# Performance work log

Measured on AMD Instinct MI355X. Metric: run time of the kernel, lower is better.

The kernel has to match this reference:

```python
import jax, jax.numpy as jnp
import numpy as np

# LIF hyperparameters (match init_kwargs)
DT = 1.0
TAU = 20.0
THRESHOLD = 1.0
RESET = 0.0
REST = 0.0
REFR_PERIOD = 2.0
LOW_BOUND = -1.0
KOEFF = float(np.exp(-DT / TAU))  # membrane decay per step
N = 2048
N_IN = 512
N_OUT = 256
B = 64
T = 512


def setup_inputs() -> dict:
    key = jax.random.key(0)
    k1, k2 = jax.random.split(key)
    # Binary input spike trains [B, n_in, T] (uint8 semantics, stored as float32)
    inp = (jax.random.uniform(k1, (B, N_IN, T)) < 0.2).astype(jnp.float32)
    # Dense synaptic weight matrix W [N, N]; row i = incoming weights of neuron i
    W = jax.random.normal(k2, (N, N), dtype=jnp.float32) * (0.1 / np.sqrt(N))
    return {"inp": inp, "W": W}


def reference(inp, W):
    batch, n_in, time = inp.shape
    n = W.shape[0]
    xs = jnp.moveaxis(inp, 2, 0)  # [T, B, n_in]

    def step(carry, x_t):
        state, refr, out_t = carry  # state/refr/out_t: [B, N]
        # Inject input spikes into the first n_in output slots
        out_t = out_t.at[:, :n_in].set(x_t)
        # LIF update: decay toward rest + synaptic input W @ out_t
        state = (state - REST) * KOEFF + REST + jnp.einsum('ij,bj->bi', W, out_t)
        # Refractory neurons clamped to reset potential
        state = jnp.where(refr > 0, RESET, state)
        spike = state >= THRESHOLD
        refr = refr - DT
        refr = jnp.where(spike, REFR_PERIOD, refr)
        # Lower-bound clamp on membrane potential
        state = jnp.where(state < LOW_BOUND, LOW_BOUND, state)
        out_t = spike.astype(jnp.float32)
        return (state, refr, out_t), out_t[:, -N_OUT:]

    init = (jnp.zeros((batch, n), jnp.float32),
            jnp.zeros((batch, n), jnp.float32),
            jnp.zeros((batch, n), jnp.float32))
    _, outs = jax.lax.scan(step, init, xs)  # outs: [T, B, n_out]
    return jnp.transpose(outs, (1, 2, 0))  # [B, n_out, T]
```

## Files before the change

### kernel.cpp

```cpp
#include <hip/hip_runtime.h>

#define KOEFF 0.951229424500714f
#define K64   0.040762204f

typedef unsigned short u16;
typedef __attribute__((ext_vector_type(8))) short short8;
typedef __attribute__((ext_vector_type(4))) float f32x4;

__device__ __forceinline__ u16 f2bf(float f) {
  unsigned int v = __float_as_uint(f);
  unsigned int r = (v + 0x7FFFu + ((v >> 16) & 1u)) >> 16;
  return (u16)r;
}
__device__ __forceinline__ float bf2f(u16 u) {
  return __uint_as_float(((unsigned int)u) << 16);
}

__global__ __launch_bounds__(256) void k_xt(const float* __restrict__ X, u16* __restrict__ XT) {
  __shared__ float tile[64][65];
  const int b  = blockIdx.z;
  const int j0 = blockIdx.x * 64;
  const int t0 = blockIdx.y * 64;
  const float* src = X + ((size_t)b * 512 + j0) * 512 + t0;
  for (int e = threadIdx.x; e < 64 * 16; e += 256) {
    int r = e >> 4, c = e & 15;
    float4 v = *(const float4*)(src + (size_t)r * 512 + c * 4);
    tile[r][c * 4 + 0] = v.x; tile[r][c * 4 + 1] = v.y;
    tile[r][c * 4 + 2] = v.z; tile[r][c * 4 + 3] = v.w;
  }
  __syncthreads();
  u16* dst = XT + ((size_t)b * 512 + t0) * 512 + j0;
  for (int e = threadIdx.x; e < 64 * 16; e += 256) {
    int tr = e >> 4, c = e & 15;
    ushort4 o;
    o.x = f2bf(tile[c * 4 + 0][tr]); o.y = f2bf(tile[c * 4 + 1][tr]);
    o.z = f2bf(tile[c * 4 + 2][tr]); o.w = f2bf(tile[c * 4 + 3][tr]);
    *(ushort4*)(dst + (size_t)tr * 512 + c * 4) = o;
  }
}

__global__ __launch_bounds__(256) void k_wcvt(const float* __restrict__ W,
                                              u16* __restrict__ Whi, int* __restrict__ flags) {
  if (blockIdx.x == 0 && threadIdx.x < 64) flags[threadIdx.x] = 0;
  int p = blockIdx.x * 256 + threadIdx.x;
  if (p >= 1536 * 512) return;
  int i = p >> 9, j = p & 511;
  Whi[p] = f2bf(W[(size_t)(512 + i) * 2048 + j]);
}

__global__ __launch_bounds__(256) void k_wt2(const float* __restrict__ W, float* __restrict__ WT2) {
  __shared__ float tile[64][65];
  const int i0 = blockIdx.x * 64;
  const int j0 = blockIdx.y * 64;
  const float* src = W + (size_t)(512 + i0) * 2048 + 512 + j0;
  for (int e = threadIdx.x; e < 64 * 16; e += 256) {
    int r = e >> 4, c = e & 15;
    float4 v = *(const float4*)(src + (size_t)r * 2048 + c * 4);
    tile[r][c * 4 + 0] = v.x; tile[r][c * 4 + 1] = v.y;
    tile[r][c * 4 + 2] = v.z; tile[r][c * 4 + 3] = v.w;
  }
  __syncthreads();
  float* dst = WT2 + (size_t)j0 * 1536 + i0;
  for (int e = threadIdx.x; e < 64 * 16; e += 256) {
    int jr = e >> 4, c = e & 15;
    float4 o;
    o.x = tile[c * 4 + 0][jr]; o.y = tile[c * 4 + 1][jr];
    o.z = tile[c * 4 + 2][jr]; o.w = tile[c * 4 + 3][jr];
    *(float4*)(dst + (size_t)jr * 1536 + c * 4) = o;
  }
}

__global__ __launch_bounds__(256) void k_gemm(const u16* __restrict__ A,
                                              const u16* __restrict__ Bx, u16* __restrict__ U) {
  __shared__ u16 lA[128 * 64];
  __shared__ u16 lB[128 * 64];
  const int b    = blockIdx.y;
  const int mt   = blockIdx.x >> 2;
  const int nt   = blockIdx.x & 3;
  const int tid  = threadIdx.x;
  const int wv   = tid >> 6;
  const int lane = tid & 63;
  const int wr   = wv >> 1, wc = wv & 1;

  f32x4 acc[4][4];
#pragma unroll
  for (int mi = 0; mi < 4; ++mi)
#pragma unroll
    for (int ni = 0; ni < 4; ++ni) acc[mi][ni] = (f32x4)0.0f;

  const u16* gA = A + (size_t)mt * 128 * 512;
  const u16* gB = Bx + ((size_t)b * 512 + nt * 128) * 512;

  for (int k0 = 0; k0 < 512; k0 += 64) {
#pragma unroll
    for (int it = 0; it < 4; ++it) {
      int byteoff = wv * 4096 + it * 1024 + lane * 16;
      int row   = byteoff >> 7;
      int chunk = (byteoff >> 4) & 7;
      int ksub  = (chunk ^ (row & 7)) * 8;
      int ldsoff = wv * 2048 + it * 512;
      __builtin_amdgcn_global_load_lds(
          (const __attribute__((address_space(1))) void*)(gA + (size_t)row * 512 + k0 + ksub),
          (__attribute__((address_space(3))) void*)(lA + ldsoff), 16, 0, 0);
      __builtin_amdgcn_global_load_lds(
          (const __attribute__((address_space(1))) void*)(gB + (size_t)row * 512 + k0 + ksub),
          (__attribute__((address_space(3))) void*)(lB + ldsoff), 16, 0, 0);
    }
    __syncthreads();
#pragma unroll
    for (int kk = 0; kk < 2; ++kk) {
      short8 ah[4], bb[4];
      const int kc = kk * 4 + (lane >> 4);
      const int sw = lane & 7;
#pragma unroll
      for (int mi = 0; mi < 4; ++mi) {
        int m = wr * 64 + mi * 16 + (lane & 15);
        ah[mi] = *(const short8*)&lA[m * 64 + ((kc ^ sw) << 3)];
      }
#pragma unroll
      for (int ni = 0; ni < 4; ++ni) {
        int n = wc * 64 + ni * 16 + (lane & 15);
        bb[ni] = *(const short8*)&lB[n * 64 + ((kc ^ sw) << 3)];
      }
#pragma unroll
      for (int mi = 0; mi < 4; ++mi)
#pragma unroll
        for (int ni = 0; ni < 4; ++ni)
          acc[mi][ni] = __builtin_amdgcn_mfma_f32_16x16x32_bf16(ah[mi], bb[ni], acc[mi][ni], 0, 0, 0);
    }
    __syncthreads();
  }
#pragma unroll
  for (int mi = 0; mi < 4; ++mi) {
    int ib = mt * 128 + wr * 64 + mi * 16 + ((lane >> 4) << 2);
#pragma unroll
    for (int ni = 0; ni < 4; ++ni) {
      int t = nt * 128 + wc * 64 + ni * 16 + (lane & 15);
      f32x4 v = acc[mi][ni];
      ushort4 o;
      o.x = f2bf(v.x); o.y = f2bf(v.y); o.z = f2bf(v.z); o.w = f2bf(v.w);
      *(ushort4*)(U + ((size_t)b * 512 + t) * 1536 + ib) = o;
    }
  }
}

__global__ __launch_bounds__(256) void k_part(const u16* __restrict__ U, float* __restrict__ P) {
  const int g = blockIdx.x * 256 + threadIdx.x;
  const int i = g * 2;
  const int c = blockIdx.y, b = blockIdx.z;
  const u16* up = U + ((size_t)b * 512 + c * 64) * 1536 + i;
  float s0 = 0.f, s1 = 0.f;
  unsigned int buf[8];
#pragma unroll
  for (int j = 0; j < 8; ++j) buf[j] = *(const unsigned int*)(up + (size_t)j * 1536);
  for (int t0 = 0; t0 < 64; t0 += 8) {
#pragma unroll
    for (int j = 0; j < 8; ++j) {
      unsigned int u = buf[j];
      if (t0 + 8 < 64) buf[j] = *(const unsigned int*)(up + (size_t)(t0 + 8 + j) * 1536);
      s0 = fmaf(s0, KOEFF, bf2f((u16)(u & 0xffffu)));
      s1 = fmaf(s1, KOEFF, bf2f((u16)(u >> 16)));
    }
  }
  *(float2*)(P + ((size_t)b * 8 + c) * 1536 + i) = make_float2(s0, s1);
}

__global__ __launch_bounds__(256) void k_chunk(const u16* __restrict__ U, const float* __restrict__ P,
                                               float* __restrict__ out, int* __restrict__ flags) {
  const int g = blockIdx.x * 256 + threadIdx.x;
  const int i = g * 2;
  const int c = blockIdx.y, b = blockIdx.z;
  float s0 = 0.f, s1 = 0.f;
  const float* pp = P + (size_t)b * 8 * 1536 + i;
  for (int d = 0; d < c; ++d) {
    float2 pv = *(const float2*)(pp + (size_t)d * 1536);
    s0 = fmaf(s0, K64, pv.x);
    s1 = fmaf(s1, K64, pv.y);
  }
  const u16* up = U + ((size_t)b * 512 + c * 64) * 1536 + i;
  const bool wr = (i >= 1280);
  float* op = out + ((size_t)b * 256 + (i - 1280)) * 512 + c * 64;
  bool viol = false;
  unsigned int buf[8];
#pragma unroll
  for (int j = 0; j < 8; ++j) buf[j] = *(const unsigned int*)(up + (size_t)j * 1536);
  for (int t0 = 0; t0 < 64; t0 += 8) {
    float sp0[8], sp1[8];
#pragma unroll
    for (int j = 0; j < 8; ++j) {
      unsigned int u = buf[j];
      if (t0 + 8 < 64) buf[j] = *(const unsigned int*)(up + (size_t)(t0 + 8 + j) * 1536);
      s0 = fmaf(s0, KOEFF, bf2f((u16)(u & 0xffffu)));
      s1 = fmaf(s1, KOEFF, bf2f((u16)(u >> 16)));
      bool a = (s0 >= 1.0f), bsp = (s1 >= 1.0f);
      viol = viol || a || bsp || (s0 < -1.0f) || (s1 < -1.0f);
      sp0[j] = a ? 1.f : 0.f;
      sp1[j] = bsp ? 1.f : 0.f;
    }
    if (wr) {
      *(float4*)(op + t0)           = make_float4(sp0[0], sp0[1], sp0[2], sp0[3]);
      *(float4*)(op + t0 + 4)       = make_float4(sp0[4], sp0[5], sp0[6], sp0[7]);
      *(float4*)(op + 512 + t0)     = make_float4(sp1[0], sp1[1], sp1[2], sp1[3]);
      *(float4*)(op + 512 + t0 + 4) = make_float4(sp1[4], sp1[5], sp1[6], sp1[7]);
    }
  }
  if (viol) atomicOr(&flags[b], 1);
}

__global__ __launch_bounds__(768) void k_fix(const u16* __restrict__ U, const float* __restrict__ WT2,
                                             const int* __restrict__ flags, float* __restrict__ out) {
  const int b = blockIdx.x;
  if (flags[b] == 0) return;
  const int tid = threadIdx.x;
  const int wv = tid >> 6, lane = tid & 63;
  __shared__ unsigned long long spk[24];
  for (int w = tid; w < 24; w += 768) spk[w] = 0ULL;
  __syncthreads();
  float s0 = 0.f, s1 = 0.f, r0 = 0.f, r1 = 0.f;
  const int i0 = 2 * tid;
  const u16* ub = U + (size_t)b * 512 * 1536 + i0;
  unsigned int u = *(const unsigned int*)ub;
  for (int t = 0; t < 512; ++t) {
    unsigned int unext = u;
    if (t < 511) unext = *(const unsigned int*)(ub + (size_t)(t + 1) * 1536);
    float a0 = fmaf(s0, KOEFF, bf2f((u16)(u & 0xffffu)));
    float a1 = fmaf(s1, KOEFF, bf2f((u16)(u >> 16)));
    for (int wd = 0; wd < 24; ++wd) {
      unsigned long long m = spk[wd];
      while (m) {
        int bit = __ffsll(m) - 1;
        m &= m - 1;
        int jp = ((wd >> 1) << 7) + (bit << 1) + (wd & 1);
        float2 rv = *(const float2*)(WT2 + (size_t)jp * 1536 + i0);
        a0 += rv.x; a1 += rv.y;
      }
    }
    if (r0 > 0.f) a0 = 0.f;
    if (r1 > 0.f) a1 = 0.f;
    bool sp0 = a0 >= 1.0f, sp1 = a1 >= 1.0f;
    r0 -= 1.f; r1 -= 1.f;
    if (sp0) r0 = 2.f;
    if (sp1) r1 = 2.f;
    if (a0 < -1.f) a0 = -1.f;
    if (a1 < -1.f) a1 = -1.f;
    s0 = a0; s1 = a1;
    if (i0 >= 1280) {
      float* o = out + ((size_t)b * 256 + (i0 - 1280)) * 512 + t;
      o[0]   = sp0 ? 1.f : 0.f;
      o[512] = sp1 ? 1.f : 0.f;
    }
    __syncthreads();
    unsigned long long b0 = __ballot(sp0);
    unsigned long long b1 = __ballot(sp1);
    if (lane == 0) { spk[2 * wv] = b0; spk[2 * wv + 1] = b1; }
    __syncthreads();
    u = unext;
  }
}

__global__ __launch_bounds__(256) void k_wtf(const float* __restrict__ W, float* __restrict__ WTF) {
  __shared__ float tile[64][65];
  const int i0 = blockIdx.x * 64;
  const int j0 = blockIdx.y * 64;
  const float* src = W + (size_t)(512 + i0) * 2048 + j0;
  for (int e = threadIdx.x; e < 64 * 16; e += 256) {
    int r = e >> 4, c = e & 15;
    float4 v = *(const float4*)(src + (size_t)r * 2048 + c * 4);
    tile[r][c * 4 + 0] = v.x; tile[r][c * 4 + 1] = v.y;
    tile[r][c * 4 + 2] = v.z; tile[r][c * 4 + 3] = v.w;
  }
  __syncthreads();
  float* dst = WTF + (size_t)j0 * 1536 + i0;
  for (int e = threadIdx.x; e < 64 * 16; e += 256) {
    int jr = e >> 4, c = e & 15;
    float4 o;
    o.x = tile[c * 4 + 0][jr]; o.y = tile[c * 4 + 1][jr];
    o.z = tile[c * 4 + 2][jr]; o.w = tile[c * 4 + 3][jr];
    *(float4*)(dst + (size_t)jr * 1536 + c * 4) = o;
  }
}

__global__ __launch_bounds__(256) void k_exact(const float* __restrict__ X, const float* __restrict__ W,
                                               const float* __restrict__ WTF, int use_wt,
                                               float* __restrict__ out) {
  const int b = blockIdx.x, tid = threadIdx.x;
  const int wv = tid >> 6, lane = tid & 63;
  float st[6], rf[6];
#pragma unroll
  for (int r = 0; r < 6; ++r) { st[r] = 0.f; rf[r] = 0.f; }
  __shared__ unsigned int mask[64];
  for (int w = tid; w < 64; w += 256) mask[w] = 0u;
  __syncthreads();
  for (int t = 0; t < 512; ++t) {
    {
      float x = X[((size_t)b * 512 + tid) * 512 + t];
      unsigned long long bl = __ballot(x > 0.5f);
      if (lane == 0) { mask[2 * wv] = (unsigned int)bl; mask[2 * wv + 1] = (unsigned int)(bl >> 32); }
      x = X[((size_t)b * 512 + 256 + tid) * 512 + t];
      bl = __ballot(x > 0.5f);
      if (lane == 0) { mask[8 + 2 * wv] = (unsigned int)bl; mask[9 + 2 * wv] = (unsigned int)(bl >> 32); }
    }
    __syncthreads();
    float add[6] = {0.f, 0.f, 0.f, 0.f, 0.f, 0.f};
    for (int wd = 0; wd < 64; ++wd) {
      unsigned int m = mask[wd];
      while (m) {
        int bitp = __ffs(m) - 1;
        m &= m - 1;
        int j = wd * 32 + bitp;
        if (use_wt) {
          const float* row = WTF + (size_t)j * 1536;
#pragma unroll
          for (int r = 0; r < 6; ++r) add[r] += row[tid + 256 * r];
        } else {
#pragma unroll
          for (int r = 0; r < 6; ++r) add[r] += W[(size_t)(512 + tid + 256 * r) * 2048 + j];
        }
      }
    }
    bool sp[6];
#pragma unroll
    for (int r = 0; r < 6; ++r) {
      float a = fmaf(st[r], KOEFF, add[r]);
      if (rf[r] > 0.f) a = 0.f;
      sp[r] = a >= 1.0f;
      rf[r] -= 1.f;
      if (sp[r]) rf[r] = 2.f;
      if (a < -1.f) a = -1.f;
      st[r] = a;
      int gi = 512 + tid + 256 * r;
      if (gi >= 1792) out[((size_t)b * 256 + (gi - 1792)) * 512 + t] = sp[r] ? 1.f : 0.f;
    }
    __syncthreads();
#pragma unroll
    for (int r = 0; r < 6; ++r) {
      unsigned long long bl = __ballot(sp[r]);
      if (lane == 0) {
        mask[16 + 8 * r + 2 * wv] = (unsigned int)bl;
        mask[17 + 8 * r + 2 * wv] = (unsigned int)(bl >> 32);
      }
    }
    __syncthreads();
  }
}

extern "C" void kernel_launch(void* const* d_in, const int* in_sizes, int n_in,
                              void* d_out, int out_size, void* d_ws, size_t ws_size,
                              hipStream_t stream) {
  const float* X = (const float*)d_in[0];
  const float* W = (const float*)d_in[1];
  float* out = (float*)d_out;
  char* ws = (char*)d_ws;

  const size_t SZ_XT  = 64ull * 512 * 512 * 2;
  const size_t SZ_WH  = 1536ull * 512 * 2;
  const size_t SZ_WT2 = 1536ull * 1536 * 4;
  const size_t SZ_U   = 64ull * 512 * 1536 * 2;
  const size_t SZ_P   = 64ull * 8 * 1536 * 4;
  const size_t SZ_FL  = 256;
  const size_t NEED_FULL = SZ_XT + SZ_WH + SZ_WT2 + SZ_U + SZ_P + SZ_FL;
  const size_t NEED_MID  = 2048ull * 1536 * 4;

  if (ws_size >= NEED_FULL) {
    u16*   XT  = (u16*)ws;
    u16*   Whi = (u16*)(ws + SZ_XT);
    float* WT2 = (float*)(ws + SZ_XT + SZ_WH);
    u16*   U   = (u16*)(ws + SZ_XT + SZ_WH + SZ_WT2);
    float* P   = (float*)(ws + SZ_XT + SZ_WH + SZ_WT2 + SZ_U);
    int*   FL  = (int*)(ws + SZ_XT + SZ_WH + SZ_WT2 + SZ_U + SZ_P);
    k_xt<<<dim3(8, 8, 64), 256, 0, stream>>>(X, XT);
    k_wcvt<<<3072, 256, 0, stream>>>(W, Whi, FL);
    k_wt2<<<dim3(24, 24), 256, 0, stream>>>(W, WT2);
    k_gemm<<<dim3(48, 64), 256, 0, stream>>>(Whi, XT, U);
    k_part<<<dim3(3, 8, 64), 256, 0, stream>>>(U, P);
    k_chunk<<<dim3(3, 8, 64), 256, 0, stream>>>(U, P, out, FL);
    k_fix<<<64, 768, 0, stream>>>(U, WT2, FL, out);
  } else if (ws_size >= NEED_MID) {
    float* WTF = (float*)ws;
    k_wtf<<<dim3(24, 32), 256, 0, stream>>>(W, WTF);
    k_exact<<<64, 256, 0, stream>>>(X, W, WTF, 1, out);
  } else {
    k_exact<<<64, 256, 0, stream>>>(X, W, nullptr, 0, out);
  }
}
```

Measured before the change: 252.0 us.

## Fuse prep kernels into one launch and compute chunk partials in GEMM epilogue

Merges the three preprocessing kernels (input transpose, weight bf16 conversion, weight transpose) into a single launch that dispatches on block index. It also drops the separate partial-sum kernel: the GEMM epilogue computes each 64-step chunk's decayed sum directly from the fp32 accumulators, using exp2-based decay weights and a 16-lane shuffle reduction. This removes three launches and a full re-read of the bf16 U buffer. The trade-offs are a heavier GEMM epilogue and partials that now come from the fp32 accumulators instead of the rounded bf16 values, which slightly changes numerics.

Measured after the change: 237.4 us. -5.8%, faster.

```diff
diff --git a/kernel.cpp b/kernel.cpp
--- a/kernel.cpp
+++ b/kernel.cpp
@@ -2,6 +2,7 @@
 
 #define KOEFF 0.951229424500714f
 #define K64   0.040762204f
+#define LOG2K (-0.07213475204444817f)
 
 typedef unsigned short u16;
 typedef __attribute__((ext_vector_type(8))) short short8;
@@ -16,62 +17,63 @@
   return __uint_as_float(((unsigned int)u) << 16);
 }
 
-__global__ __launch_bounds__(256) void k_xt(const float* __restrict__ X, u16* __restrict__ XT) {
+__global__ __launch_bounds__(256) void k_prep(const float* __restrict__ X, const float* __restrict__ W,
+                                              u16* __restrict__ XT, u16* __restrict__ Whi,
+                                              float* __restrict__ WT2, int* __restrict__ flags) {
   __shared__ float tile[64][65];
-  const int b  = blockIdx.z;
-  const int j0 = blockIdx.x * 64;
-  const int t0 = blockIdx.y * 64;
-  const float* src = X + ((size_t)b * 512 + j0) * 512 + t0;
-  for (int e = threadIdx.x; e < 64 * 16; e += 256) {
-    int r = e >> 4, c = e & 15;
-    float4 v = *(const float4*)(src + (size_t)r * 512 + c * 4);
-    tile[r][c * 4 + 0] = v.x; tile[r][c * 4 + 1] = v.y;
-    tile[r][c * 4 + 2] = v.z; tile[r][c * 4 + 3] = v.w;
-  }
-  __syncthreads();
-  u16* dst = XT + ((size_t)b * 512 + t0) * 512 + j0;
-  for (int e = threadIdx.x; e < 64 * 16; e += 256) {
-    int tr = e >> 4, c = e & 15;
-    ushort4 o;
-    o.x = f2bf(tile[c * 4 + 0][tr]); o.y = f2bf(tile[c * 4 + 1][tr]);
-    o.z = f2bf(tile[c * 4 + 2][tr]); o.w = f2bf(tile[c * 4 + 3][tr]);
-    *(ushort4*)(dst + (size_t)tr * 512 + c * 4) = o;
-  }
-}
-
-__global__ __launch_bounds__(256) void k_wcvt(const float* __restrict__ W,
-                                              u16* __restrict__ Whi, int* __restrict__ flags) {
-  if (blockIdx.x == 0 && threadIdx.x < 64) flags[threadIdx.x] = 0;
-  int p = blockIdx.x * 256 + threadIdx.x;
-  if (p >= 1536 * 512) return;
-  int i = p >> 9, j = p & 511;
-  Whi[p] = f2bf(W[(size_t)(512 + i) * 2048 + j]);
-}
-
-__global__ __launch_bounds__(256) void k_wt2(const float* __restrict__ W, float* __restrict__ WT2) {
-  __shared__ float tile[64][65];
-  const int i0 = blockIdx.x * 64;
-  const int j0 = blockIdx.y * 64;
-  const float* src = W + (size_t)(512 + i0) * 2048 + 512 + j0;
-  for (int e = threadIdx.x; e < 64 * 16; e += 256) {
-    int r = e >> 4, c = e & 15;
-    float4 v = *(const float4*)(src + (size_t)r * 2048 + c * 4);
-    tile[r][c * 4 + 0] = v.x; tile[r][c * 4 + 1] = v.y;
-    tile[r][c * 4 + 2] = v.z; tile[r][c * 4 + 3] = v.w;
-  }
-  __syncthreads();
-  float* dst = WT2 + (size_t)j0 * 1536 + i0;
-  for (int e = threadIdx.x; e < 64 * 16; e += 256) {
-    int jr = e >> 4, c = e & 15;
-    float4 o;
-    o.x = tile[c * 4 + 0][jr]; o.y = tile[c * 4 + 1][jr];
-    o.z = tile[c * 4 + 2][jr]; o.w = tile[c * 4 + 3][jr];
-    *(float4*)(dst + (size_t)jr * 1536 + c * 4) = o;
+  const int blk = blockIdx.x;
+  if (blk < 4096) {
+    const int b  = blk >> 6;
+    const int r2 = blk & 63;
+    const int j0 = (r2 & 7) * 64;
+    const int t0 = (r2 >> 3) * 64;
+    const float* src = X + ((size_t)b * 512 + j0) * 512 + t0;
+    for (int e = threadIdx.x; e < 64 * 16; e += 256) {
+      int r = e >> 4, c = e & 15;
+      float4 v = *(const float4*)(src + (size_t)r * 512 + c * 4);
+      tile[r][c * 4 + 0] = v.x; tile[r][c * 4 + 1] = v.y;
+      tile[r][c * 4 + 2] = v.z; tile[r][c * 4 + 3] = v.w;
+    }
+    __syncthreads();
+    u16* dst = XT + ((size_t)b * 512 + t0) * 512 + j0;
+    for (int e = threadIdx.x; e < 64 * 16; e += 256) {
+      int tr = e >> 4, c = e & 15;
+      ushort4 o;
+      o.x = f2bf(tile[c * 4 + 0][tr]); o.y = f2bf(tile[c * 4 + 1][tr]);
+      o.z = f2bf(tile[c * 4 + 2][tr]); o.w = f2bf(tile[c * 4 + 3][tr]);
+      *(ushort4*)(dst + (size_t)tr * 512 + c * 4) = o;
+    }
+  } else if (blk < 7168) {
+    if (blk == 4096 && threadIdx.x < 64) flags[threadIdx.x] = 0;
+    int p = (blk - 4096) * 256 + threadIdx.x;
+    int i = p >> 9, j = p & 511;
+    Whi[p] = f2bf(W[(size_t)(512 + i) * 2048 + j]);
+  } else {
+    const int bx = blk - 7168;
+    const int i0 = (bx / 24) * 64;
+    const int j0 = (bx % 24) * 64;
+    const float* src = W + (size_t)(512 + i0) * 2048 + 512 + j0;
+    for (int e = threadIdx.x; e < 64 * 16; e += 256) {
+      int r = e >> 4, c = e & 15;
+      float4 v = *(const float4*)(src + (size_t)r * 2048 + c * 4);
+      tile[r][c * 4 + 0] = v.x; tile[r][c * 4 + 1] = v.y;
+      tile[r][c * 4 + 2] = v.z; tile[r][c * 4 + 3] = v.w;
+    }
+    __syncthreads();
+    float* dst = WT2 + (size_t)j0 * 1536 + i0;
+    for (int e = threadIdx.x; e < 64 * 16; e += 256) {
+      int jr = e >> 4, c = e & 15;
+      float4 o;
+      o.x = tile[c * 4 + 0][jr]; o.y = tile[c * 4 + 1][jr];
+      o.z = tile[c * 4 + 2][jr]; o.w = tile[c * 4 + 3][jr];
+      *(float4*)(dst + (size_t)jr * 1536 + c * 4) = o;
+    }
   }
 }
 
 __global__ __launch_bounds__(256) void k_gemm(const u16* __restrict__ A,
-                                              const u16* __restrict__ Bx, u16* __restrict__ U) {
+                                              const u16* __restrict__ Bx, u16* __restrict__ U,
+                                              float* __restrict__ P) {
   __shared__ u16 lA[128 * 64];
   __shared__ u16 lB[128 * 64];
   const int b    = blockIdx.y;
@@ -142,27 +144,42 @@
       *(ushort4*)(U + ((size_t)b * 512 + t) * 1536 + ib) = o;
     }
   }
-}
-
-__global__ __launch_bounds__(256) void k_part(const u16* __restrict__ U, float* __restrict__ P) {
-  const int g = blockIdx.x * 256 + threadIdx.x;
-  const int i = g * 2;
-  const int c = blockIdx.y, b = blockIdx.z;
-  const u16* up = U + ((size_t)b * 512 + c * 64) * 1536 + i;
-  float s0 = 0.f, s1 = 0.f;
-  unsigned int buf[8];
-#pragma unroll
-  for (int j = 0; j < 8; ++j) buf[j] = *(const unsigned int*)(up + (size_t)j * 1536);
-  for (int t0 = 0; t0 < 64; t0 += 8) {
-#pragma unroll
-    for (int j = 0; j < 8; ++j) {
-      unsigned int u = buf[j];
-      if (t0 + 8 < 64) buf[j] = *(const unsigned int*)(up + (size_t)(t0 + 8 + j) * 1536);
-      s0 = fmaf(s0, KOEFF, bf2f((u16)(u & 0xffffu)));
-      s1 = fmaf(s1, KOEFF, bf2f((u16)(u >> 16)));
-    }
-  }
-  *(float2*)(P + ((size_t)b * 8 + c) * 1536 + i) = make_float2(s0, s1);
+  {
+    const int tl = lane & 15;
+    const int c  = nt * 2 + wc;
+    float pv[4][4];
+#pragma unroll
+    for (int mi = 0; mi < 4; ++mi)
+#pragma unroll
+      for (int q = 0; q < 4; ++q) pv[mi][q] = 0.f;
+#pragma unroll
+    for (int ni = 0; ni < 4; ++ni) {
+      float w = exp2f(LOG2K * (float)(63 - ni * 16 - tl));
+#pragma unroll
+      for (int mi = 0; mi < 4; ++mi) {
+        f32x4 a = acc[mi][ni];
+        pv[mi][0] = fmaf(w, a.x, pv[mi][0]);
+        pv[mi][1] = fmaf(w, a.y, pv[mi][1]);
+        pv[mi][2] = fmaf(w, a.z, pv[mi][2]);
+        pv[mi][3] = fmaf(w, a.w, pv[mi][3]);
+      }
+    }
+#pragma unroll
+    for (int off = 1; off < 16; off <<= 1)
+#pragma unroll
+      for (int mi = 0; mi < 4; ++mi)
+#pragma unroll
+        for (int q = 0; q < 4; ++q)
+          pv[mi][q] += __shfl_xor(pv[mi][q], off, 16);
+    if (tl == 0) {
+      int ib = mt * 128 + wr * 64 + ((lane >> 4) << 2);
+      float* pb = P + ((size_t)b * 8 + c) * 1536 + ib;
+#pragma unroll
+      for (int mi = 0; mi < 4; ++mi)
+#pragma unroll
+        for (int q = 0; q < 4; ++q) pb[mi * 16 + q] = pv[mi][q];
+    }
+  }
 }
 
 __global__ __launch_bounds__(256) void k_chunk(const u16* __restrict__ U, const float* __restrict__ P,
@@ -368,11 +385,8 @@
     u16*   U   = (u16*)(ws + SZ_XT + SZ_WH + SZ_WT2);
     float* P   = (float*)(ws + SZ_XT + SZ_WH + SZ_WT2 + SZ_U);
     int*   FL  = (int*)(ws + SZ_XT + SZ_WH + SZ_WT2 + SZ_U + SZ_P);
-    k_xt<<<dim3(8, 8, 64), 256, 0, stream>>>(X, XT);
-    k_wcvt<<<3072, 256, 0, stream>>>(W, Whi, FL);
-    k_wt2<<<dim3(24, 24), 256, 0, stream>>>(W, WT2);
-    k_gemm<<<dim3(48, 64), 256, 0, stream>>>(Whi, XT, U);
-    k_part<<<dim3(3, 8, 64), 256, 0, stream>>>(U, P);
+    k_prep<<<7744, 256, 0, stream>>>(X, W, XT, Whi, WT2, FL);
+    k_gemm<<<dim3(48, 64), 256, 0, stream>>>(Whi, XT, U, P);
     k_chunk<<<dim3(3, 8, 64), 256, 0, stream>>>(U, P, out, FL);
     k_fix<<<64, 768, 0, stream>>>(U, WT2, FL, out);
   } else if (ws_size >= NEED_MID) {
```
